# Kernel tuning notes

Measured on AMD Instinct MI355X. Metric: run time of the kernel, lower is better.

## Reference

```python
import jax, jax.numpy as jnp
import numpy as np

HIDDEN = 51
LW = LH = 7


def setup_inputs() -> dict:
    key = jax.random.key(0)
    ks = jax.random.split(key, 14)
    N, T = 256, 2000
    s = lambda k, shape, fan_in: jax.random.uniform(k, shape, jnp.float32, -1.0, 1.0) / np.sqrt(fan_in)
    inp = {
        "stimulus": jax.random.normal(ks[0], (N, T, LH, LW), jnp.float32),
        # linear_layer: Linear(49 -> 1)
        "Wl": s(ks[1], (1, LW * LH), LW * LH),
        "bl": s(ks[2], (1,), LW * LH),
        # first_lstm: LSTMCell(1 -> 51)
        "Wih1": s(ks[3], (4 * HIDDEN, 1), HIDDEN),
        "Whh1": s(ks[4], (4 * HIDDEN, HIDDEN), HIDDEN),
        "bih1": s(ks[5], (4 * HIDDEN,), HIDDEN),
        "bhh1": s(ks[6], (4 * HIDDEN,), HIDDEN),
        # second_lstm: LSTMCell(51 -> 1)
        "Wih2": s(ks[7], (4 * 1, HIDDEN), 1),
        "Whh2": s(ks[8], (4 * 1, 1), 1),
        "bih2": s(ks[9], (4 * 1,), 1),
        "bhh2": s(ks[10], (4 * 1,), 1),
        # adjust_layer: Linear(1 -> 1)
        "Wa": s(ks[11], (1, 1), 1),
        "ba": s(ks[12], (1,), 1),
    }
    return inp


def _lstm_cell(x, h, c, Wih, Whh, bih, bhh):
    # PyTorch LSTMCell: gates order i, f, g, o
    gates = x @ Wih.T + bih + h @ Whh.T + bhh
    i, f, g, o = jnp.split(gates, 4, axis=-1)
    i = jax.nn.sigmoid(i)
    f = jax.nn.sigmoid(f)
    g = jnp.tanh(g)
    o = jax.nn.sigmoid(o)
    c_new = f * c + i * g
    h_new = o * jnp.tanh(c_new)
    return h_new, c_new


def reference(stimulus, Wl, bl, Wih1, Whh1, bih1, bhh1, Wih2, Whh2, bih2, bhh2, Wa, ba):
    N, T = stimulus.shape[0], stimulus.shape[1]
    x = stimulus.reshape(N, T, LW * LH)
    # Time-independent input projection + ReLU, done once for all steps: (N, T, 1)
    x_lin = jax.nn.relu(jnp.einsum("ntf,of->nto", x, Wl) + bl)

    h1_0 = jnp.zeros((N, HIDDEN), stimulus.dtype)
    c1_0 = jnp.zeros((N, HIDDEN), stimulus.dtype)
    h2_0 = jnp.zeros((N, 1), stimulus.dtype)
    c2_0 = jnp.zeros((N, 1), stimulus.dtype)

    def step(carry, xt):
        h1, c1, h2, c2 = carry
        h1, c1 = _lstm_cell(xt, h1, c1, Wih1, Whh1, bih1, bhh1)
        h2, c2 = _lstm_cell(h1, h2, c2, Wih2, Whh2, bih2, bhh2)
        out = h2 @ Wa.T + ba  # (N, 1)
        return (h1, c1, h2, c2), out[:, 0]

    xs = jnp.swapaxes(x_lin, 0, 1)  # (T, N, 1)
    _, outs = jax.lax.scan(step, (h1_0, c1_0, h2_0, c2_0), xs)
    return jnp.swapaxes(outs, 0, 1)  # (N, T)
```

## Files before the change

kernel.cpp:

```cpp
#include <hip/hip_runtime.h>

#define T_STEPS 2000
#define NBATCH  256
#define HID     51
#define FEAT    49
#define ROWF4   784
#define XTOT4   (NBATCH * T_STEPS * FEAT / 4)
#define PSTRIDE 5

typedef _Float16 v2h __attribute__((ext_vector_type(2)));

__device__ __forceinline__ float rl(float v, int lane) {
    return __int_as_float(__builtin_amdgcn_readlane(__float_as_int(v), lane));
}
__device__ __forceinline__ int rli(int v, int lane) {
    return __builtin_amdgcn_readlane(v, lane);
}
__device__ __forceinline__ float sigmoidf_fast(float x) {
    return __builtin_amdgcn_rcpf(1.0f + __builtin_amdgcn_exp2f(-1.4426950408889634f * x));
}
__device__ __forceinline__ float tanhf_fast(float x) {
    return 1.0f - 2.0f * __builtin_amdgcn_rcpf(1.0f + __builtin_amdgcn_exp2f(2.8853900817779268f * x));
}
__device__ __forceinline__ int packh2(float lo, float hi) {
    v2h p = (v2h){(_Float16)lo, (_Float16)hi};
    return __builtin_bit_cast(int, p);
}
__device__ __forceinline__ float dot2(int w, int h, float acc) {
    return __builtin_amdgcn_fdot2(__builtin_bit_cast(v2h, w),
                                  __builtin_bit_cast(v2h, h), acc, false);
}
__device__ __forceinline__ void bar_lds() {
    asm volatile("s_waitcnt lgkmcnt(0)" ::: "memory");
    __builtin_amdgcn_s_barrier();
    asm volatile("" ::: "memory");
}
__device__ __forceinline__ float row_dot(const float* row, const float* __restrict__ Wl) {
    float a0 = 0, a1 = 0, a2 = 0, a3 = 0, a4 = 0, a5 = 0, a6 = 0;
#pragma unroll
    for (int j = 0; j < FEAT; j += 7) {
        a0 = fmaf(row[j    ], Wl[j    ], a0);
        a1 = fmaf(row[j + 1], Wl[j + 1], a1);
        a2 = fmaf(row[j + 2], Wl[j + 2], a2);
        a3 = fmaf(row[j + 3], Wl[j + 3], a3);
        a4 = fmaf(row[j + 4], Wl[j + 4], a4);
        a5 = fmaf(row[j + 5], Wl[j + 5], a5);
        a6 = fmaf(row[j + 6], Wl[j + 6], a6);
    }
    return ((a0 + a1) + (a2 + a3)) + ((a4 + a5) + a6);
}

#define REP26(F) F(0) F(1) F(2) F(3) F(4) F(5) F(6) F(7) F(8) F(9) F(10) F(11) F(12) \
                 F(13) F(14) F(15) F(16) F(17) F(18) F(19) F(20) F(21) F(22) F(23) F(24) F(25)

__global__ __attribute__((amdgpu_flat_work_group_size(256, 256), amdgpu_waves_per_eu(1)))
void rnn_kernel(
    const float* __restrict__ x,
    const float* __restrict__ Wl, const float* __restrict__ bl,
    const float* __restrict__ Wih1, const float* __restrict__ Whh1,
    const float* __restrict__ bih1, const float* __restrict__ bhh1,
    const float* __restrict__ Wih2, const float* __restrict__ Whh2,
    const float* __restrict__ bih2, const float* __restrict__ bhh2,
    const float* __restrict__ Wa, const float* __restrict__ ba,
    float* __restrict__ out)
{
    const int n    = blockIdx.x;
    const int tid  = threadIdx.x;
    const int wid  = tid >> 6;
    const int lane = tid & 63;
    float* optr = out + (size_t)n * T_STEPS;
    const float4* x4 = (const float4*)x;
    const int sbase = n * (T_STEPS * FEAT / 4);

    __shared__ float xt_[64 * FEAT];
    __shared__ float pt[2][64 * PSTRIDE];
    __shared__ float ob[64];
    float4* t4 = (float4*)xt_;

#define DECLW(j) int w_##j; int sh_##j;
    REP26(DECLW)
    {
        const float* srow;
        float msk;
        if (lane < HID) { srow = Whh1 + (wid * HID + lane) * HID; msk = 1.0f; }
        else            { srow = Wih2 + wid * HID; msk = (lane == HID) ? 1.0f : 0.0f; }
        const float wh2 = Whh2[wid] * ((lane == HID) ? 1.0f : 0.0f);
#define LOADW(j) { \
        float lo = srow[2*(j)] * msk; \
        float hi = (2*(j)+1 < HID) ? srow[2*(j)+1] * msk : wh2; \
        w_##j = packh2(lo, hi); \
        asm("" : "+v"(w_##j)); }
        REP26(LOADW)
    }

    float wx = 0.0f, b = 0.0f;
    if (lane < HID) {
        wx = Wih1[wid * HID + lane];
        b  = bih1[wid * HID + lane] + bhh1[wid * HID + lane];
    } else if (lane == HID) {
        b  = bih2[wid] + bhh2[wid];
    }
    const float wav = Wa[0], bav = ba[0];
    const float bl0 = bl[0];

#define INITS(j) sh_##j = 0;
    REP26(INITS)

    float c = 0.0f, h = 0.0f;

    float4 p0, p1, p2, p3;
#define PF(base) { \
        int g0_ = (base) + tid;       g0_ = g0_ < XTOT4 ? g0_ : (XTOT4 - 1); p0 = x4[g0_]; \
        int g1_ = (base) + 256 + tid; g1_ = g1_ < XTOT4 ? g1_ : (XTOT4 - 1); p1 = x4[g1_]; \
        int g2_ = (base) + 512 + tid; g2_ = g2_ < XTOT4 ? g2_ : (XTOT4 - 1); p2 = x4[g2_]; \
        if (tid < 16) { int g3_ = (base) + 768 + tid; g3_ = g3_ < XTOT4 ? g3_ : (XTOT4 - 1); p3 = x4[g3_]; } }
#define COMMIT { t4[tid] = p0; t4[tid + 256] = p1; t4[tid + 512] = p2; \
                 if (tid < 16) t4[tid + 768] = p3; }
#define ROWDOT(dst) { float d_ = row_dot(&xt_[lane * FEAT], Wl); \
                      dst = fmaxf(d_ + bl0, 0.0f); }

    float xa, xb;
    PF(sbase)              COMMIT  bar_lds();  ROWDOT(xa)
    PF(sbase + ROWF4)      bar_lds();  COMMIT  bar_lds();  ROWDOT(xb)
    PF(sbase + 2 * ROWF4)

    const int prow = lane * PSTRIDE;

#pragma unroll 1
    for (int t = 0; t <= T_STEPS; ++t) {
        if ((t & 63) == 0 && t > 0 && t < T_STEPS) {
            const int k = t >> 6;
            if (wid == 0) {
                int oi = 64 * (k - 1) - 1 + lane;
                float ov = ob[lane];
                if (oi >= 0) optr[oi] = ov;
            }
            xa = xb;
            COMMIT
            bar_lds();
            ROWDOT(xb)
            PF(sbase + (k + 2) * ROWF4)
        }
        float xt = rl(xa, t & 63);

        float aA = fmaf(wx, xt, b), aB = 0.0f;
#define DOT(j) { if ((j) & 1) aB = dot2(w_##j, sh_##j, aB); \
                 else         aA = dot2(w_##j, sh_##j, aA); }
        REP26(DOT)
        float a = aA + aB;

        float act = (wid == 2) ? tanhf_fast(a) : sigmoidf_fast(a);

        float* ptw = pt[t & 1];
        ptw[prow + wid] = act;
        bar_lds();
        float ig = ptw[prow + 0];
        float fg = ptw[prow + 1];
        float gg = ptw[prow + 2];
        float og = ptw[prow + 3];

        c = fmaf(fg, c, ig * gg);
        h = og * tanhf_fast(c);
        if (t == 0 && lane >= HID) { c = 0.0f; h = 0.0f; }

        if (wid == 0 && lane == HID && t > 0)
            ob[t & 63] = fmaf(h, wav, bav);

        int hz = (int)(unsigned)__builtin_bit_cast(unsigned short, (_Float16)h);
        int nb = __builtin_amdgcn_mov_dpp(hz, 0xB1, 0xF, 0xF, true);
        int pair = hz | (nb << 16);
#define BCAST(j) sh_##j = rli(pair, 2 * (j));
        REP26(BCAST)
    }

    if (wid == 0 && lane <= 16) optr[1983 + lane] = ob[lane];
}

extern "C" void kernel_launch(void* const* d_in, const int* in_sizes, int n_in,
                              void* d_out, int out_size, void* d_ws, size_t ws_size,
                              hipStream_t stream) {
    const float* x    = (const float*)d_in[0];
    const float* Wl   = (const float*)d_in[1];
    const float* bl   = (const float*)d_in[2];
    const float* Wih1 = (const float*)d_in[3];
    const float* Whh1 = (const float*)d_in[4];
    const float* bih1 = (const float*)d_in[5];
    const float* bhh1 = (const float*)d_in[6];
    const float* Wih2 = (const float*)d_in[7];
    const float* Whh2 = (const float*)d_in[8];
    const float* bih2 = (const float*)d_in[9];
    const float* bhh2 = (const float*)d_in[10];
    const float* Wa   = (const float*)d_in[11];
    const float* ba   = (const float*)d_in[12];
    float* out = (float*)d_out;

    rnn_kernel<<<NBATCH, 256, 0, stream>>>(x, Wl, bl, Wih1, Whh1, bih1, bhh1,
                                           Wih2, Whh2, bih2, bhh2, Wa, ba, out);
}
```

Before: 874.3 us.

## Pack two batch samples per 512-thread block to share a CU

Each block now processes two independent batch samples, with separate LDS buffers per sample, and the grid is halved to 128 blocks. The intent is to put two waves on each SIMD so that the latency of one sample's serial recurrence can be hidden by the other's. In exchange, only half the CUs are used, and the per-step barrier now synchronizes eight waves across both samples, coupling their progress.

```diff
diff --git a/kernel.cpp b/kernel.cpp
--- a/kernel.cpp
+++ b/kernel.cpp
@@ -53,7 +53,7 @@
 #define REP26(F) F(0) F(1) F(2) F(3) F(4) F(5) F(6) F(7) F(8) F(9) F(10) F(11) F(12) \
                  F(13) F(14) F(15) F(16) F(17) F(18) F(19) F(20) F(21) F(22) F(23) F(24) F(25)
 
-__global__ __attribute__((amdgpu_flat_work_group_size(256, 256), amdgpu_waves_per_eu(1)))
+__global__ __attribute__((amdgpu_flat_work_group_size(512, 512), amdgpu_waves_per_eu(2)))
 void rnn_kernel(
     const float* __restrict__ x,
     const float* __restrict__ Wl, const float* __restrict__ bl,
@@ -64,18 +64,20 @@
     const float* __restrict__ Wa, const float* __restrict__ ba,
     float* __restrict__ out)
 {
-    const int n    = blockIdx.x;
     const int tid  = threadIdx.x;
-    const int wid  = tid >> 6;
+    const int samp = tid >> 8;
+    const int stid = tid & 255;
+    const int wid  = stid >> 6;
     const int lane = tid & 63;
+    const int n    = blockIdx.x * 2 + samp;
     float* optr = out + (size_t)n * T_STEPS;
     const float4* x4 = (const float4*)x;
     const int sbase = n * (T_STEPS * FEAT / 4);
 
-    __shared__ float xt_[64 * FEAT];
-    __shared__ float pt[2][64 * PSTRIDE];
-    __shared__ float ob[64];
-    float4* t4 = (float4*)xt_;
+    __shared__ float xt_[2][64 * FEAT];
+    __shared__ float pt[2][2][64 * PSTRIDE];
+    __shared__ float ob[2][64];
+    float4* t4s = (float4*)xt_[samp];
 
 #define DECLW(j) int w_##j; int sh_##j;
     REP26(DECLW)
@@ -110,13 +112,13 @@
 
     float4 p0, p1, p2, p3;
 #define PF(base) { \
-        int g0_ = (base) + tid;       g0_ = g0_ < XTOT4 ? g0_ : (XTOT4 - 1); p0 = x4[g0_]; \
-        int g1_ = (base) + 256 + tid; g1_ = g1_ < XTOT4 ? g1_ : (XTOT4 - 1); p1 = x4[g1_]; \
-        int g2_ = (base) + 512 + tid; g2_ = g2_ < XTOT4 ? g2_ : (XTOT4 - 1); p2 = x4[g2_]; \
-        if (tid < 16) { int g3_ = (base) + 768 + tid; g3_ = g3_ < XTOT4 ? g3_ : (XTOT4 - 1); p3 = x4[g3_]; } }
-#define COMMIT { t4[tid] = p0; t4[tid + 256] = p1; t4[tid + 512] = p2; \
-                 if (tid < 16) t4[tid + 768] = p3; }
-#define ROWDOT(dst) { float d_ = row_dot(&xt_[lane * FEAT], Wl); \
+        int g0_ = (base) + stid;       g0_ = g0_ < XTOT4 ? g0_ : (XTOT4 - 1); p0 = x4[g0_]; \
+        int g1_ = (base) + 256 + stid; g1_ = g1_ < XTOT4 ? g1_ : (XTOT4 - 1); p1 = x4[g1_]; \
+        int g2_ = (base) + 512 + stid; g2_ = g2_ < XTOT4 ? g2_ : (XTOT4 - 1); p2 = x4[g2_]; \
+        if (stid < 16) { int g3_ = (base) + 768 + stid; g3_ = g3_ < XTOT4 ? g3_ : (XTOT4 - 1); p3 = x4[g3_]; } }
+#define COMMIT { t4s[stid] = p0; t4s[stid + 256] = p1; t4s[stid + 512] = p2; \
+                 if (stid < 16) t4s[stid + 768] = p3; }
+#define ROWDOT(dst) { float d_ = row_dot(&xt_[samp][lane * FEAT], Wl); \
                       dst = fmaxf(d_ + bl0, 0.0f); }
 
     float xa, xb;
@@ -132,7 +134,7 @@
             const int k = t >> 6;
             if (wid == 0) {
                 int oi = 64 * (k - 1) - 1 + lane;
-                float ov = ob[lane];
+                float ov = ob[samp][lane];
                 if (oi >= 0) optr[oi] = ov;
             }
             xa = xb;
@@ -151,7 +153,7 @@
 
         float act = (wid == 2) ? tanhf_fast(a) : sigmoidf_fast(a);
 
-        float* ptw = pt[t & 1];
+        float* ptw = pt[samp][t & 1];
         ptw[prow + wid] = act;
         bar_lds();
         float ig = ptw[prow + 0];
@@ -164,7 +166,7 @@
         if (t == 0 && lane >= HID) { c = 0.0f; h = 0.0f; }
 
         if (wid == 0 && lane == HID && t > 0)
-            ob[t & 63] = fmaf(h, wav, bav);
+            ob[samp][t & 63] = fmaf(h, wav, bav);
 
         int hz = (int)(unsigned)__builtin_bit_cast(unsigned short, (_Float16)h);
         int nb = __builtin_amdgcn_mov_dpp(hz, 0xB1, 0xF, 0xF, true);
@@ -173,7 +175,7 @@
         REP26(BCAST)
     }
 
-    if (wid == 0 && lane <= 16) optr[1983 + lane] = ob[lane];
+    if (wid == 0 && lane <= 16) optr[1983 + lane] = ob[samp][lane];
 }
 
 extern "C" void kernel_launch(void* const* d_in, const int* in_sizes, int n_in,
@@ -194,6 +196,6 @@
     const float* ba   = (const float*)d_in[12];
     float* out = (float*)d_out;
 
-    rnn_kernel<<<NBATCH, 256, 0, stream>>>(x, Wl, bl, Wih1, Whh1, bih1, bhh1,
-                                           Wih2, Whh2, bih2, bhh2, Wa, ba, out);
-}
+    rnn_kernel<<<NBATCH / 2, 512, 0, stream>>>(x, Wl, bl, Wih1, Whh1, bih1, bhh1,
+                                               Wih2, Whh2, bih2, bhh2, Wa, ba, out);
+}
```

Result: slower. 1.127 ms (+28.9%).

## Split recurrent dot product across two wave teams with partial-sum reduction

Applied to the files above, without the earlier changes.

Doubles the block to 512 threads so two teams of four gate-waves each compute half of the 51-wide recurrent dot product. Partial sums go through LDS, and the first team reduces them, applies the activations and publishes the gates through a second LDS buffer. This is meant to shorten the serial dot2/readlane chain per timestep, at the cost of an extra barrier and LDS round trip per step and two waves sharing each SIMD.

```diff
diff --git a/kernel.cpp b/kernel.cpp
--- a/kernel.cpp
+++ b/kernel.cpp
@@ -6,7 +6,8 @@
 #define FEAT    49
 #define ROWF4   784
 #define XTOT4   (NBATCH * T_STEPS * FEAT / 4)
-#define PSTRIDE 5
+#define PSTR    9
+#define ASTR    5
 
 typedef _Float16 v2h __attribute__((ext_vector_type(2)));
 
@@ -50,10 +51,9 @@
     return ((a0 + a1) + (a2 + a3)) + ((a4 + a5) + a6);
 }
 
-#define REP26(F) F(0) F(1) F(2) F(3) F(4) F(5) F(6) F(7) F(8) F(9) F(10) F(11) F(12) \
-                 F(13) F(14) F(15) F(16) F(17) F(18) F(19) F(20) F(21) F(22) F(23) F(24) F(25)
-
-__global__ __attribute__((amdgpu_flat_work_group_size(256, 256), amdgpu_waves_per_eu(1)))
+#define REP13(F) F(0) F(1) F(2) F(3) F(4) F(5) F(6) F(7) F(8) F(9) F(10) F(11) F(12)
+
+__global__ __attribute__((amdgpu_flat_work_group_size(512, 512), amdgpu_waves_per_eu(2)))
 void rnn_kernel(
     const float* __restrict__ x,
     const float* __restrict__ Wl, const float* __restrict__ bl,
@@ -67,55 +67,60 @@
     const int n    = blockIdx.x;
     const int tid  = threadIdx.x;
     const int wid  = tid >> 6;
+    const int gate = wid & 3;
+    const int team = wid >> 2;
     const int lane = tid & 63;
+    const int kb   = 13 * team;
     float* optr = out + (size_t)n * T_STEPS;
     const float4* x4 = (const float4*)x;
     const int sbase = n * (T_STEPS * FEAT / 4);
 
     __shared__ float xt_[64 * FEAT];
-    __shared__ float pt[2][64 * PSTRIDE];
+    __shared__ float pt[2][64 * PSTR];
+    __shared__ float at[2][64 * ASTR];
     __shared__ float ob[64];
     float4* t4 = (float4*)xt_;
 
 #define DECLW(j) int w_##j; int sh_##j;
-    REP26(DECLW)
+    REP13(DECLW)
     {
         const float* srow;
         float msk;
-        if (lane < HID) { srow = Whh1 + (wid * HID + lane) * HID; msk = 1.0f; }
-        else            { srow = Wih2 + wid * HID; msk = (lane == HID) ? 1.0f : 0.0f; }
-        const float wh2 = Whh2[wid] * ((lane == HID) ? 1.0f : 0.0f);
+        if (lane < HID) { srow = Whh1 + (gate * HID + lane) * HID; msk = 1.0f; }
+        else            { srow = Wih2 + gate * HID; msk = (lane == HID) ? 1.0f : 0.0f; }
+        const float wh2 = Whh2[gate] * ((lane == HID) ? 1.0f : 0.0f);
 #define LOADW(j) { \
-        float lo = srow[2*(j)] * msk; \
-        float hi = (2*(j)+1 < HID) ? srow[2*(j)+1] * msk : wh2; \
+        const int jj = kb + (j); \
+        float lo = srow[2 * jj] * msk; \
+        float hi = (2 * jj + 1 < HID) ? srow[2 * jj + 1] * msk : wh2; \
         w_##j = packh2(lo, hi); \
         asm("" : "+v"(w_##j)); }
-        REP26(LOADW)
+        REP13(LOADW)
     }
 
     float wx = 0.0f, b = 0.0f;
-    if (lane < HID) {
-        wx = Wih1[wid * HID + lane];
-        b  = bih1[wid * HID + lane] + bhh1[wid * HID + lane];
-    } else if (lane == HID) {
-        b  = bih2[wid] + bhh2[wid];
+    if (team == 0) {
+        if (lane < HID) {
+            wx = Wih1[gate * HID + lane];
+            b  = bih1[gate * HID + lane] + bhh1[gate * HID + lane];
+        } else if (lane == HID) {
+            b  = bih2[gate] + bhh2[gate];
+        }
     }
     const float wav = Wa[0], bav = ba[0];
     const float bl0 = bl[0];
 
 #define INITS(j) sh_##j = 0;
-    REP26(INITS)
+    REP13(INITS)
 
     float c = 0.0f, h = 0.0f;
 
-    float4 p0, p1, p2, p3;
+    float4 p0, p1;
 #define PF(base) { \
-        int g0_ = (base) + tid;       g0_ = g0_ < XTOT4 ? g0_ : (XTOT4 - 1); p0 = x4[g0_]; \
-        int g1_ = (base) + 256 + tid; g1_ = g1_ < XTOT4 ? g1_ : (XTOT4 - 1); p1 = x4[g1_]; \
-        int g2_ = (base) + 512 + tid; g2_ = g2_ < XTOT4 ? g2_ : (XTOT4 - 1); p2 = x4[g2_]; \
-        if (tid < 16) { int g3_ = (base) + 768 + tid; g3_ = g3_ < XTOT4 ? g3_ : (XTOT4 - 1); p3 = x4[g3_]; } }
-#define COMMIT { t4[tid] = p0; t4[tid + 256] = p1; t4[tid + 512] = p2; \
-                 if (tid < 16) t4[tid + 768] = p3; }
+        int g0_ = (base) + tid; g0_ = g0_ < XTOT4 ? g0_ : (XTOT4 - 1); p0 = x4[g0_]; \
+        if (tid < ROWF4 - 512) { int g1_ = (base) + 512 + tid; \
+            g1_ = g1_ < XTOT4 ? g1_ : (XTOT4 - 1); p1 = x4[g1_]; } }
+#define COMMIT { t4[tid] = p0; if (tid < ROWF4 - 512) t4[tid + 512] = p1; }
 #define ROWDOT(dst) { float d_ = row_dot(&xt_[lane * FEAT], Wl); \
                       dst = fmaxf(d_ + bl0, 0.0f); }
 
@@ -124,13 +129,14 @@
     PF(sbase + ROWF4)      bar_lds();  COMMIT  bar_lds();  ROWDOT(xb)
     PF(sbase + 2 * ROWF4)
 
-    const int prow = lane * PSTRIDE;
+    const int prow = lane * PSTR;
+    const int arow = lane * ASTR;
 
 #pragma unroll 1
     for (int t = 0; t <= T_STEPS; ++t) {
         if ((t & 63) == 0 && t > 0 && t < T_STEPS) {
             const int k = t >> 6;
-            if (wid == 0) {
+            if (wid == 4) {
                 int oi = 64 * (k - 1) - 1 + lane;
                 float ov = ob[lane];
                 if (oi >= 0) optr[oi] = ov;
@@ -146,34 +152,42 @@
         float aA = fmaf(wx, xt, b), aB = 0.0f;
 #define DOT(j) { if ((j) & 1) aB = dot2(w_##j, sh_##j, aB); \
                  else         aA = dot2(w_##j, sh_##j, aA); }
-        REP26(DOT)
+        REP13(DOT)
         float a = aA + aB;
 
-        float act = (wid == 2) ? tanhf_fast(a) : sigmoidf_fast(a);
-
         float* ptw = pt[t & 1];
-        ptw[prow + wid] = act;
+        ptw[prow + wid] = a;
         bar_lds();
-        float ig = ptw[prow + 0];
-        float fg = ptw[prow + 1];
-        float gg = ptw[prow + 2];
-        float og = ptw[prow + 3];
-
+
+        float* atw = at[t & 1];
+        if (wid < 4) {
+            float pA = ptw[prow + gate];
+            float pB = ptw[prow + 4 + gate];
+            float s  = pA + pB;
+            float act = (gate == 2) ? tanhf_fast(s) : sigmoidf_fast(s);
+            atw[arow + gate] = act;
+        }
+        bar_lds();
+
+        float ig = atw[arow + 0];
+        float fg = atw[arow + 1];
+        float gg = atw[arow + 2];
+        float og = atw[arow + 3];
         c = fmaf(fg, c, ig * gg);
         h = og * tanhf_fast(c);
         if (t == 0 && lane >= HID) { c = 0.0f; h = 0.0f; }
 
-        if (wid == 0 && lane == HID && t > 0)
+        if (wid == 4 && lane == HID && t > 0)
             ob[t & 63] = fmaf(h, wav, bav);
 
         int hz = (int)(unsigned)__builtin_bit_cast(unsigned short, (_Float16)h);
         int nb = __builtin_amdgcn_mov_dpp(hz, 0xB1, 0xF, 0xF, true);
         int pair = hz | (nb << 16);
-#define BCAST(j) sh_##j = rli(pair, 2 * (j));
-        REP26(BCAST)
-    }
-
-    if (wid == 0 && lane <= 16) optr[1983 + lane] = ob[lane];
+#define BCAST(j) sh_##j = rli(pair, 2 * (kb + (j)));
+        REP13(BCAST)
+    }
+
+    if (wid == 4 && lane <= 16) optr[1983 + lane] = ob[lane];
 }
 
 extern "C" void kernel_launch(void* const* d_in, const int* in_sizes, int n_in,
@@ -194,6 +208,6 @@
     const float* ba   = (const float*)d_in[12];
     float* out = (float*)d_out;
 
-    rnn_kernel<<<NBATCH, 256, 0, stream>>>(x, Wl, bl, Wih1, Whh1, bih1, bhh1,
+    rnn_kernel<<<NBATCH, 512, 0, stream>>>(x, Wl, bl, Wih1, Whh1, bih1, bhh1,
                                            Wih2, Whh2, bih2, bhh2, Wa, ba, out);
 }
```

Result: slower. 1.341 ms (+53.4%).
